# Kernel tuning notes

Measured on AMD Instinct MI355X. Metric: run time of the kernel, lower is better.

The kernel has to match this reference:

```python
import jax, jax.numpy as jnp
import numpy as np

SLOPE = 25.0  # snntorch surrogate.fast_sigmoid default slope
THR = 1.0
BETA = 0.5
NUM_HEADS = 8

@jax.custom_vjp
def spike(u):
    # forward: heaviside; backward: fast-sigmoid surrogate
    return (u > 0).astype(u.dtype)

def _spike_fwd(u):
    return (u > 0).astype(u.dtype), u

def _spike_bwd(u, g):
    return (g / (SLOPE * jnp.abs(u) + 1.0) ** 2,)

spike.defvjp(_spike_fwd, _spike_bwd)

def lif(inp, mem):
    # snntorch Leaky, reset_mechanism='subtract': reset from previous mem (detached)
    reset = jax.lax.stop_gradient((mem > THR).astype(mem.dtype))
    mem_new = BETA * mem + inp - reset * THR
    spk = spike(mem_new - THR)
    return spk, mem_new

def conv1x1(x, W):
    # nn.Conv2d(C,C,1,bias=False): pure channel matmul
    return jnp.einsum('bihw,oi->bohw', x, W)

def setup_inputs():
    key = jax.random.key(0)
    ks = jax.random.split(key, 5)
    B, C, H, W = 8, 256, 64, 64
    x = jax.random.normal(ks[0], (B, C, H, W), jnp.float32)
    z = jnp.zeros((B, C, H, W), jnp.float32)
    s = 1.0 / np.sqrt(C)
    Wq = jax.random.normal(ks[1], (C, C), jnp.float32) * s
    Wk = jax.random.normal(ks[2], (C, C), jnp.float32) * s
    Wv = jax.random.normal(ks[3], (C, C), jnp.float32) * s
    Wo = jax.random.normal(ks[4], (C, C), jnp.float32) * s
    gamma = jnp.ones((C,), jnp.float32)
    beta_bn = jnp.zeros((C,), jnp.float32)
    return {'x': x, 'q_mem': z, 'k_mem': z, 'v_mem': z,
            'Wq': Wq, 'Wk': Wk, 'Wv': Wv, 'Wo': Wo,
            'gamma': gamma, 'beta_bn': beta_bn}

def reference(x, q_mem, k_mem, v_mem, Wq, Wk, Wv, Wo, gamma, beta_bn):
    B, C, H, W = x.shape
    N = H * W
    hd = C // NUM_HEADS
    scale = hd ** -0.5

    q_spk, q_mem_n = lif(conv1x1(x, Wq), q_mem)
    k_spk, k_mem_n = lif(conv1x1(x, Wk), k_mem)
    v_spk, v_mem_n = lif(conv1x1(x, Wv), v_mem)

    # bipolar spikes in {-1,+1}, reshape to (B, h, N, d)
    def to_heads(s):
        t = (2.0 * s - 1.0).reshape(B, NUM_HEADS, hd, N)
        return jnp.transpose(t, (0, 1, 3, 2))

    q = jax.nn.elu(to_heads(q_spk)) + 1.0
    k = jax.nn.elu(to_heads(k_spk)) + 1.0
    v = to_heads(v_spk)

    kv = jnp.einsum('bhnd,bhne->bhde', k, v)            # (B,h,d,d)
    out = jnp.einsum('bhnd,bhde->bhne', q, kv) * scale  # (B,h,N,d)
    k_sum = jnp.sum(k, axis=2)                          # (B,h,d)
    denom = jnp.einsum('bhnd,bhd->bhn', q, k_sum) + 1e-6
    out = out / denom[..., None]

    out = jnp.transpose(out, (0, 1, 3, 2)).reshape(B, C, H, W)
    out = conv1x1(out, Wo)

    # BatchNorm2d, training mode (biased batch stats), eps=1e-5
    mean = jnp.mean(out, axis=(0, 2, 3), keepdims=True)
    var = jnp.var(out, axis=(0, 2, 3), keepdims=True)
    out = (out - mean) / jnp.sqrt(var + 1e-5)
    out = out * gamma[None, :, None, None] + beta_bn[None, :, None, None]

    return (out, q_mem_n, k_mem_n, v_mem_n)
```

## Files before the change

### kernel.cpp

```cpp
#include <hip/hip_runtime.h>

#define B_ 8
#define C_ 256
#define N_ 4096
#define HD_ 32

#define ALPHA_ 0.36787944117144233f
#define BETAS_ (2.0f - ALPHA_)
#define SCALE_ 0.17677669529663687f

typedef _Float16 f16;
typedef _Float16 f16x8 __attribute__((ext_vector_type(8)));
typedef float f32x4 __attribute__((ext_vector_type(4)));
typedef unsigned long long u64;
typedef __attribute__((address_space(3))) f16 lds_f16;

#define MFMA(a,b,c) __builtin_amdgcn_mfma_f32_16x16x32_f16((a),(b),(c),0,0,0)

#define GLDS(g, l) __builtin_amdgcn_global_load_lds( \
    (const __attribute__((address_space(1))) void*)(g), \
    (__attribute__((address_space(3))) void*)(l), 16, 0, 0)

#define DSR(dst, off) asm volatile("ds_read_b128 %0, %1" : "=v"(dst) : "v"(off))

template<int N> __device__ __forceinline__ void wait_vmcnt() {
    if constexpr (N == 0)       asm volatile("s_waitcnt vmcnt(0)" ::: "memory");
    else if constexpr (N == 2)  asm volatile("s_waitcnt vmcnt(2)" ::: "memory");
    else if constexpr (N == 4)  asm volatile("s_waitcnt vmcnt(4)" ::: "memory");
    else if constexpr (N == 8)  asm volatile("s_waitcnt vmcnt(8)" ::: "memory");
    else if constexpr (N == 16) asm volatile("s_waitcnt vmcnt(16)" ::: "memory");
}

__global__ __launch_bounds__(256) void transpose_split(
    const float* __restrict__ x, f16* __restrict__ XTh, f16* __restrict__ XTl)
{
    __shared__ float tile[32][257];
    int t = threadIdx.x;
    int b = blockIdx.z, i0 = blockIdx.y * 32, n0 = blockIdx.x * 256;
    const float* src = x + ((size_t)b * C_ + i0) * N_ + n0;
    int r = t >> 3, c0 = (t & 7) * 32;
    #pragma unroll
    for (int q = 0; q < 8; ++q) {
        float4 v = *reinterpret_cast<const float4*>(src + (size_t)r * N_ + c0 + q * 4);
        tile[r][c0 + q*4 + 0] = v.x; tile[r][c0 + q*4 + 1] = v.y;
        tile[r][c0 + q*4 + 2] = v.z; tile[r][c0 + q*4 + 3] = v.w;
    }
    __syncthreads();
    size_t ob = ((size_t)b * N_ + n0 + t) * C_ + i0;
    #pragma unroll
    for (int q = 0; q < 4; ++q) {
        f16x8 hv, lv;
        #pragma unroll
        for (int j = 0; j < 8; ++j) {
            float v = tile[q*8 + j][t];
            f16 h = (f16)v;
            hv[j] = h;
            lv[j] = (f16)(v - (float)h);
        }
        *reinterpret_cast<f16x8*>(XTh + ob + q*8) = hv;
        *reinterpret_cast<f16x8*>(XTl + ob + q*8) = lv;
    }
}

__global__ __launch_bounds__(256) void weight_split(
    const float* __restrict__ Wq, const float* __restrict__ Wk,
    const float* __restrict__ Wv, const float* __restrict__ Wo,
    f16* __restrict__ Wch, f16* __restrict__ Wcl)
{
    int idx4 = (blockIdx.x * 256 + threadIdx.x) * 4;
    int o = idx4 >> 8, i = idx4 & 255;
    const float* src = (o < 256) ? (Wq + (size_t)o * 256)
                     : (o < 512) ? (Wk + (size_t)(o - 256) * 256)
                     : (o < 768) ? (Wv + (size_t)(o - 512) * 256)
                                 : (Wo + (size_t)(o - 768) * 256);
    float4 v = *reinterpret_cast<const float4*>(src + i);
    f16 h0 = (f16)v.x, h1 = (f16)v.y, h2 = (f16)v.z, h3 = (f16)v.w;
    f16 hh[4] = { h0, h1, h2, h3 };
    f16 ll[4] = { (f16)(v.x - (float)h0), (f16)(v.y - (float)h1),
                  (f16)(v.z - (float)h2), (f16)(v.w - (float)h3) };
    *reinterpret_cast<uint2*>(Wch + idx4) = *reinterpret_cast<uint2*>(hh);
    *reinterpret_cast<uint2*>(Wcl + idx4) = *reinterpret_cast<uint2*>(ll);
}

template<bool LIF, bool FULLP>
__global__ __launch_bounds__(256, 3) void mfma_gemm(
    const f16* __restrict__ Wch, const f16* __restrict__ Wcl,
    const f16* __restrict__ Bh,  const f16* __restrict__ Bl,
    const float* __restrict__ mq, const float* __restrict__ mk2,
    const float* __restrict__ mv,
    float* __restrict__ o0, float* __restrict__ o1, float* __restrict__ o2,
    u64* __restrict__ rowAll)
{
    constexpr int SLOTS = FULLP ? 1024 : 512;
    constexpr int NGL   = FULLP ? 4 : 2;

    int gid = blockIdx.x;
    int b = gid & 7, slot = gid >> 3;
    int conv, oTi, nt;
    if (LIF) { conv = slot % 3; int rest = slot / 3; oTi = rest & 1; nt = rest >> 1; }
    else     { conv = 0;        oTi = slot & 1;      nt = slot >> 1; }
    int wRow0 = (LIF ? conv * 256 : 768) + oTi * 128;
    int chOut0 = oTi * 128;
    int nT = nt * 128;

    const float* memP = nullptr; float* outP; u64* rowP = nullptr;
    if (LIF) {
        memP = (conv == 0) ? mq : (conv == 1) ? mk2 : mv;
        outP = (conv == 0) ? o0 : (conv == 1) ? o1 : o2;
        rowP = rowAll + (size_t)conv * (8 * 256 * 64);
    } else outP = o0;

    __shared__ __align__(16) f16 smem[3][SLOTS * 8];

    int t = threadIdx.x;
    int wid = t >> 6, lane = t & 63;
    int wm = wid >> 1, wn = wid & 1;
    int lr = lane & 15, g = lane >> 4;

    const f16* gB[NGL];
    #pragma unroll
    for (int i = 0; i < NGL; ++i) {
        int s = i * 256 + t;
        int sp = s & 511;
        int r = sp >> 2, c = (sp & 3) ^ ((r >> 1) & 3);
        const f16* plane = (s < 512) ? Bh : Bl;
        gB[i] = plane + ((size_t)b * N_ + nT + r) * 256 + c * 8;
    }

    int aOff[4];
    #pragma unroll
    for (int m = 0; m < 4; ++m)
        aOff[m] = (wRow0 + wm * 64 + m * 16 + lr) * 256 + g * 8;

    unsigned lbase = (unsigned)(size_t)(lds_f16*)&smem[0][0];
    unsigned offB[4];
    #pragma unroll
    for (int n = 0; n < 4; ++n) {
        int r = wn * 64 + n * 16 + lr;
        offB[n] = (unsigned)((r * 4 + (g ^ ((r >> 1) & 3))) * 16);
    }

    f32x4 acc[4][4];
    #pragma unroll
    for (int m = 0; m < 4; ++m)
        #pragma unroll
        for (int n = 0; n < 4; ++n) acc[m][n] = (f32x4){0.f, 0.f, 0.f, 0.f};

    #pragma unroll
    for (int i = 0; i < NGL; ++i) GLDS(gB[i],      &smem[0][(i * 256 + t) * 8]);
    #pragma unroll
    for (int i = 0; i < NGL; ++i) GLDS(gB[i] + 32, &smem[1][(i * 256 + t) * 8]);
    wait_vmcnt<NGL>();
    __builtin_amdgcn_s_barrier();
    __builtin_amdgcn_sched_barrier(0);

#define GEMM_STEP(KS) do { \
    constexpr int ks = (KS); \
    f16x8 ah[4], al[4]; \
    _Pragma("unroll") \
    for (int m = 0; m < 4; ++m) { \
        ah[m] = *reinterpret_cast<const f16x8*>(Wch + aOff[m] + ks * 32); \
        if (FULLP) al[m] = *reinterpret_cast<const f16x8*>(Wcl + aOff[m] + ks * 32); \
    } \
    __builtin_amdgcn_sched_barrier(0); \
    if constexpr (ks < 6) { \
        _Pragma("unroll") \
        for (int i = 0; i < NGL; ++i) \
            GLDS(gB[i] + (ks + 2) * 32, &smem[(ks + 2) % 3][(i * 256 + t) * 8]); \
    } \
    __builtin_amdgcn_sched_barrier(0); \
    const unsigned base = lbase + (unsigned)((ks % 3) * (SLOTS * 16)); \
    f16x8 bhf[4], blf[4]; \
    _Pragma("unroll") \
    for (int n = 0; n < 4; ++n) { \
        DSR(bhf[n], base + offB[n]); \
        if (FULLP) DSR(blf[n], base + offB[n] + 8192); \
    } \
    asm volatile("s_waitcnt lgkmcnt(0)" ::: "memory"); \
    __builtin_amdgcn_sched_barrier(0); \
    wait_vmcnt<(ks < 6) ? (FULLP ? 4 : 2) : 0>();   \
    __builtin_amdgcn_sched_barrier(0); \
    _Pragma("unroll") \
    for (int n = 0; n < 4; ++n) \
        _Pragma("unroll") \
        for (int m = 0; m < 4; ++m) { \
            acc[m][n] = MFMA(ah[m], bhf[n], acc[m][n]); \
            if (FULLP) { \
                acc[m][n] = MFMA(ah[m], blf[n], acc[m][n]); \
                acc[m][n] = MFMA(al[m], bhf[n], acc[m][n]); \
            } \
        } \
    __builtin_amdgcn_sched_barrier(0); \
    __builtin_amdgcn_s_barrier(); \
    __builtin_amdgcn_sched_barrier(0); \
} while (0)

    GEMM_STEP(0); GEMM_STEP(1); GEMM_STEP(2); GEMM_STEP(3);
    GEMM_STEP(4); GEMM_STEP(5); GEMM_STEP(6); GEMM_STEP(7);
#undef GEMM_STEP

    if (LIF) {
        #pragma unroll
        for (int m = 0; m < 4; ++m) {
            int oLoc = chOut0 + wm * 64 + m * 16 + g * 4;
            u64 rw0 = 0, rw1 = 0, rw2 = 0, rw3 = 0;
            #pragma unroll
            for (int n = 0; n < 4; ++n) {
                int nn = nT + wn * 64 + n * 16 + lr;
                #pragma unroll
                for (int r = 0; r < 4; ++r) {
                    size_t idx = ((size_t)b * C_ + oLoc + r) * N_ + nn;
                    float mm = memP[idx];
                    float v = 0.5f * mm + acc[m][n][r] - (mm > 1.0f ? 1.0f : 0.0f);
                    outP[idx] = v;
                    u64 bl = __ballot(v > 1.0f);
                    u64 fld = ((bl >> (g * 16)) & 0xFFFFull) << (n * 16);
                    if (r == 0) rw0 |= fld; else if (r == 1) rw1 |= fld;
                    else if (r == 2) rw2 |= fld; else rw3 |= fld;
                }
            }
            if (lr == 0) {
                size_t rb = ((size_t)b * 256 + oLoc) * 64 + (nt * 2 + wn);
                rowP[rb]       = rw0;
                rowP[rb + 64]  = rw1;
                rowP[rb + 128] = rw2;
                rowP[rb + 192] = rw3;
            }
        }
    } else {
        #pragma unroll
        for (int m = 0; m < 4; ++m) {
            int oLoc = chOut0 + wm * 64 + m * 16 + g * 4;
            #pragma unroll
            for (int n = 0; n < 4; ++n) {
                int nn = nT + wn * 64 + n * 16 + lr;
                #pragma unroll
                for (int r = 0; r < 4; ++r) {
                    size_t idx = ((size_t)b * C_ + oLoc + r) * N_ + nn;
                    outP[idx] = acc[m][n][r];
                }
            }
        }
    }
}

__global__ __launch_bounds__(256) void kv_stage1(
    const u64* __restrict__ krow, const u64* __restrict__ vrow,
    int* __restrict__ pkv, int* __restrict__ pck, int* __restrict__ pcv)
{
    int bh = blockIdx.x, sl = blockIdx.y;
    int b = bh >> 3, h = bh & 7;
    __shared__ u64 kr[32][9], vr[32][9];
    int t = threadIdx.x;
    {
        int d = t >> 3, w = t & 7;
        size_t a = ((size_t)b * 256 + h * HD_ + d) * 64 + sl * 8 + w;
        kr[d][w] = krow[a];
        vr[d][w] = vrow[a];
    }
    __syncthreads();

    int base = bh * 8 + sl;
    if (t < 32) {
        int c = 0;
        #pragma unroll
        for (int w = 0; w < 8; ++w) c += __popcll(kr[t][w]);
        pck[base * 32 + t] = c;
    } else if (t < 64) {
        int dd = t - 32, c = 0;
        #pragma unroll
        for (int w = 0; w < 8; ++w) c += __popcll(vr[dd][w]);
        pcv[base * 32 + dd] = c;
    }
    int d = t >> 3, e0 = (t & 7) * 4;
    #pragma unroll
    for (int j = 0; j < 4; ++j) {
        int e = e0 + j, P = 0;
        #pragma unroll
        for (int w = 0; w < 8; ++w) P += __popcll(kr[d][w] & vr[e][w]);
        pkv[(size_t)base * 1024 + d * 32 + e] = P;
    }
}

__global__ __launch_bounds__(256) void kv_stage2(
    const int* __restrict__ pkv, const int* __restrict__ pck,
    const int* __restrict__ pcv, float* __restrict__ kvp, float* __restrict__ ksump)
{
    int bh = blockIdx.x, t = threadIdx.x;
    __shared__ float ck[32], cv[32];
    if (t < 32) {
        int s = 0;
        #pragma unroll
        for (int sl = 0; sl < 8; ++sl) s += pck[(bh * 8 + sl) * 32 + t];
        ck[t] = (float)s;
    } else if (t < 64) {
        int dd = t - 32, s = 0;
        #pragma unroll
        for (int sl = 0; sl < 8; ++sl) s += pcv[(bh * 8 + sl) * 32 + dd];
        cv[dd] = (float)s;
    }
    __syncthreads();
    int d = t >> 3, e0 = (t & 7) * 4;
    #pragma unroll
    for (int j = 0; j < 4; ++j) {
        int e = e0 + j, P = 0;
        #pragma unroll
        for (int sl = 0; sl < 8; ++sl) P += pkv[(size_t)(bh * 8 + sl) * 1024 + d * 32 + e];
        float skv = 2.0f * (float)P - ck[d];
        float sv  = 2.0f * cv[e] - 4096.0f;
        kvp[(size_t)bh * 1024 + d * 32 + e] = ALPHA_ * sv + BETAS_ * skv;
    }
    if ((t & 7) == 0)
        ksump[bh * 32 + d] = ALPHA_ * 4096.0f + BETAS_ * ck[d];
}

__global__ __launch_bounds__(256) void att_kernel(
    const u64* __restrict__ qrow, const float* __restrict__ kvp,
    const float* __restrict__ ksump, f16* __restrict__ ATh)
{
    int bh = blockIdx.y; int b = bh >> 3, h = bh & 7;
    int n0 = blockIdx.x * 256;

    __shared__ u64 qw[32][5];
    int t = threadIdx.x;
    if (t < 128) {
        int d2 = t >> 2, w4 = t & 3;
        qw[d2][w4] = qrow[((size_t)b * 256 + h * HD_ + d2) * 64 + (n0 >> 6) + w4];
    }
    __syncthreads();

    float q[32];
    #pragma unroll
    for (int d2 = 0; d2 < 32; ++d2)
        q[d2] = ((qw[d2][t >> 6] >> (t & 63)) & 1) ? 2.0f : ALPHA_;

    const float* ksb = ksump + bh * 32;
    float den = 1e-6f;
    #pragma unroll
    for (int d2 = 0; d2 < 32; ++d2) den += q[d2] * ksb[d2];
    float rden = SCALE_ / den;

    const float* kvb = kvp + (size_t)bh * 1024;
    size_t ob = ((size_t)b * N_ + n0 + t) * C_ + h * HD_;
    #pragma unroll
    for (int qq = 0; qq < 4; ++qq) {
        f16x8 hv;
        #pragma unroll
        for (int j = 0; j < 8; ++j) {
            int e = qq * 8 + j;
            float num = 0.0f;
            #pragma unroll
            for (int d2 = 0; d2 < 32; ++d2) num += q[d2] * kvb[d2 * 32 + e];
            hv[j] = (f16)(num * rden);
        }
        *reinterpret_cast<f16x8*>(ATh + ob + qq * 8) = hv;
    }
}

__global__ __launch_bounds__(1024) void bn_stats(
    const float* __restrict__ out2, float* __restrict__ stats)
{
    int o = blockIdx.x, t = threadIdx.x;
    double s = 0.0, ss = 0.0;
    for (int b = 0; b < B_; ++b) {
        const float* p = out2 + ((size_t)b * C_ + o) * N_;
        float4 v = *reinterpret_cast<const float4*>(&p[t * 4]);
        s  += (double)v.x + (double)v.y + (double)v.z + (double)v.w;
        ss += (double)v.x * v.x + (double)v.y * v.y + (double)v.z * v.z + (double)v.w * v.w;
    }
    __shared__ double rs[1024], rss[1024];
    rs[t] = s; rss[t] = ss;
    __syncthreads();
    for (int st = 512; st > 0; st >>= 1) {
        if (t < st) { rs[t] += rs[t + st]; rss[t] += rss[t + st]; }
        __syncthreads();
    }
    if (t == 0) {
        double mean = rs[0] / 32768.0;
        double var  = rss[0] / 32768.0 - mean * mean;
        stats[o * 2 + 0] = (float)mean;
        stats[o * 2 + 1] = (float)(1.0 / sqrt(var + 1e-5));
    }
}

__global__ __launch_bounds__(256) void bn_apply(
    float* __restrict__ out, const float* __restrict__ stats,
    const float* __restrict__ gamma, const float* __restrict__ beta)
{
    size_t i = ((size_t)blockIdx.x * 256 + threadIdx.x) * 4;
    int o = (int)((i >> 12) & 255);
    float m = stats[o * 2], r = stats[o * 2 + 1];
    float g = gamma[o] * r;
    float c = beta[o] - m * g;
    float4 v = *reinterpret_cast<float4*>(&out[i]);
    v.x = v.x * g + c; v.y = v.y * g + c;
    v.z = v.z * g + c; v.w = v.w * g + c;
    *reinterpret_cast<float4*>(&out[i]) = v;
}

extern "C" void kernel_launch(void* const* d_in, const int* in_sizes, int n_in,
                              void* d_out, int out_size, void* d_ws, size_t ws_size,
                              hipStream_t stream)
{
    (void)in_sizes; (void)n_in; (void)out_size; (void)ws_size;

    const float* x     = (const float*)d_in[0];
    const float* qmem  = (const float*)d_in[1];
    const float* kmem  = (const float*)d_in[2];
    const float* vmem  = (const float*)d_in[3];
    const float* Wq    = (const float*)d_in[4];
    const float* Wk    = (const float*)d_in[5];
    const float* Wv    = (const float*)d_in[6];
    const float* Wo    = (const float*)d_in[7];
    const float* gamma = (const float*)d_in[8];
    const float* beta  = (const float*)d_in[9];

    const size_t TSZ = (size_t)B_ * C_ * N_;
    float* out0 = (float*)d_out;
    float* outq = out0 + TSZ;
    float* outk = outq + TSZ;
    float* outv = outk + TSZ;

    const size_t RSZ = (size_t)8 * 256 * 64;
    char* w = (char*)d_ws;
    f16* XTh = (f16*)w;           w += TSZ * 2;
    f16* XTl = (f16*)w;           w += TSZ * 2;
    f16* ATh = (f16*)w;           w += TSZ * 2;
    f16* Wch = (f16*)w;           w += 1024 * 256 * 2;
    f16* Wcl = (f16*)w;           w += 1024 * 256 * 2;
    u64* rowm = (u64*)w;          w += 3 * RSZ * 8;
    int* pkv = (int*)w;           w += 64 * 8 * 1024 * 4;
    int* pck = (int*)w;           w += 64 * 8 * 32 * 4;
    int* pcv = (int*)w;           w += 64 * 8 * 32 * 4;
    float* kvp   = (float*)w;     w += 64 * 1024 * 4;
    float* ksump = (float*)w;     w += 64 * 32 * 4;
    float* stats = (float*)w;     w += 256 * 2 * 4;

    dim3 blk(256);

    transpose_split<<<dim3(16, 8, 8), blk, 0, stream>>>(x, XTh, XTl);
    weight_split<<<dim3(256), blk, 0, stream>>>(Wq, Wk, Wv, Wo, Wch, Wcl);

    mfma_gemm<true, true><<<dim3(1536), blk, 0, stream>>>(
        Wch, Wcl, XTh, XTl, qmem, kmem, vmem, outq, outk, outv, rowm);

    kv_stage1<<<dim3(64, 8), blk, 0, stream>>>(rowm + RSZ, rowm + 2 * RSZ, pkv, pck, pcv);
    kv_stage2<<<dim3(64), blk, 0, stream>>>(pkv, pck, pcv, kvp, ksump);

    att_kernel<<<dim3(16, 64), blk, 0, stream>>>(rowm, kvp, ksump, ATh);

    mfma_gemm<false, false><<<dim3(512), blk, 0, stream>>>(
        Wch, Wcl, ATh, ATh, nullptr, nullptr, nullptr, out0, nullptr, nullptr, nullptr);

    bn_stats<<<dim3(256), dim3(1024), 0, stream>>>(out0, stats);
    bn_apply<<<dim3(8192), blk, 0, stream>>>(out0, stats, gamma, beta);
}
```

Measured before the change: 184.8 us.

## Prefetch weight fragments one k-step ahead with double-buffered register loads

Weight (A) fragments were loaded synchronously from global memory at the start of each k-step. They are now loaded via inline-asm global_load_dwordx4 one step ahead into double-buffered registers, and the vmcnt waits are recounted so the A loads overlap with the LDS-staged B loads and the MFMAs. The extra register buffers raise pressure, so the occupancy hint drops from 3 to 2 blocks per SM, which risks less latency hiding from other waves. The final barrier is also dropped on the last step.

```diff
diff --git a/kernel.cpp b/kernel.cpp
--- a/kernel.cpp
+++ b/kernel.cpp
@@ -23,11 +23,17 @@
 
 #define DSR(dst, off) asm volatile("ds_read_b128 %0, %1" : "=v"(dst) : "v"(off))
 
+#define GLA(dst, ptr, ofs) asm volatile( \
+    "global_load_dwordx4 %0, %1, off offset:%c2" \
+    : "=v"(dst) : "v"(ptr), "i"(ofs))
+
 template<int N> __device__ __forceinline__ void wait_vmcnt() {
     if constexpr (N == 0)       asm volatile("s_waitcnt vmcnt(0)" ::: "memory");
     else if constexpr (N == 2)  asm volatile("s_waitcnt vmcnt(2)" ::: "memory");
     else if constexpr (N == 4)  asm volatile("s_waitcnt vmcnt(4)" ::: "memory");
+    else if constexpr (N == 6)  asm volatile("s_waitcnt vmcnt(6)" ::: "memory");
     else if constexpr (N == 8)  asm volatile("s_waitcnt vmcnt(8)" ::: "memory");
+    else if constexpr (N == 12) asm volatile("s_waitcnt vmcnt(12)" ::: "memory");
     else if constexpr (N == 16) asm volatile("s_waitcnt vmcnt(16)" ::: "memory");
 }
 
@@ -83,7 +89,7 @@
 }
 
 template<bool LIF, bool FULLP>
-__global__ __launch_bounds__(256, 3) void mfma_gemm(
+__global__ __launch_bounds__(256, 2) void mfma_gemm(
     const f16* __restrict__ Wch, const f16* __restrict__ Wcl,
     const f16* __restrict__ Bh,  const f16* __restrict__ Bl,
     const float* __restrict__ mq, const float* __restrict__ mk2,
@@ -93,6 +99,7 @@
 {
     constexpr int SLOTS = FULLP ? 1024 : 512;
     constexpr int NGL   = FULLP ? 4 : 2;
+    constexpr int NA    = FULLP ? 8 : 4;
 
     int gid = blockIdx.x;
     int b = gid & 7, slot = gid >> 3;
@@ -127,10 +134,13 @@
         gB[i] = plane + ((size_t)b * N_ + nT + r) * 256 + c * 8;
     }
 
-    int aOff[4];
-    #pragma unroll
-    for (int m = 0; m < 4; ++m)
-        aOff[m] = (wRow0 + wm * 64 + m * 16 + lr) * 256 + g * 8;
+    const f16* aPh[4]; const f16* aPl[4];
+    #pragma unroll
+    for (int m = 0; m < 4; ++m) {
+        int off = (wRow0 + wm * 64 + m * 16 + lr) * 256 + g * 8;
+        aPh[m] = Wch + off;
+        aPl[m] = Wcl + off;
+    }
 
     unsigned lbase = (unsigned)(size_t)(lds_f16*)&smem[0][0];
     unsigned offB[4];
@@ -146,8 +156,15 @@
         #pragma unroll
         for (int n = 0; n < 4; ++n) acc[m][n] = (f32x4){0.f, 0.f, 0.f, 0.f};
 
-    #pragma unroll
-    for (int i = 0; i < NGL; ++i) GLDS(gB[i],      &smem[0][(i * 256 + t) * 8]);
+    f16x8 aH[2][4], aL[2][4];
+
+    #pragma unroll
+    for (int i = 0; i < NGL; ++i) GLDS(gB[i], &smem[0][(i * 256 + t) * 8]);
+    #pragma unroll
+    for (int m = 0; m < 4; ++m) {
+        GLA(aH[0][m], aPh[m], 0);
+        if (FULLP) GLA(aL[0][m], aPl[m], 0);
+    }
     #pragma unroll
     for (int i = 0; i < NGL; ++i) GLDS(gB[i] + 32, &smem[1][(i * 256 + t) * 8]);
     wait_vmcnt<NGL>();
@@ -156,19 +173,8 @@
 
 #define GEMM_STEP(KS) do { \
     constexpr int ks = (KS); \
-    f16x8 ah[4], al[4]; \
-    _Pragma("unroll") \
-    for (int m = 0; m < 4; ++m) { \
-        ah[m] = *reinterpret_cast<const f16x8*>(Wch + aOff[m] + ks * 32); \
-        if (FULLP) al[m] = *reinterpret_cast<const f16x8*>(Wcl + aOff[m] + ks * 32); \
-    } \
-    __builtin_amdgcn_sched_barrier(0); \
-    if constexpr (ks < 6) { \
-        _Pragma("unroll") \
-        for (int i = 0; i < NGL; ++i) \
-            GLDS(gB[i] + (ks + 2) * 32, &smem[(ks + 2) % 3][(i * 256 + t) * 8]); \
-    } \
-    __builtin_amdgcn_sched_barrier(0); \
+    constexpr int cur = ks & 1, nxt = (ks + 1) & 1; \
+     \
     const unsigned base = lbase + (unsigned)((ks % 3) * (SLOTS * 16)); \
     f16x8 bhf[4], blf[4]; \
     _Pragma("unroll") \
@@ -176,23 +182,45 @@
         DSR(bhf[n], base + offB[n]); \
         if (FULLP) DSR(blf[n], base + offB[n] + 8192); \
     } \
+    __builtin_amdgcn_sched_barrier(0); \
+     \
+    if constexpr (ks < 7) { \
+        _Pragma("unroll") \
+        for (int m = 0; m < 4; ++m) { \
+            GLA(aH[nxt][m], aPh[m], (ks + 1) * 64); \
+            if (FULLP) GLA(aL[nxt][m], aPl[m], (ks + 1) * 64); \
+        } \
+    } \
+    __builtin_amdgcn_sched_barrier(0); \
+     \
+    if constexpr (ks < 6) { \
+        _Pragma("unroll") \
+        for (int i = 0; i < NGL; ++i) \
+            GLDS(gB[i] + (ks + 2) * 32, &smem[(ks + 2) % 3][(i * 256 + t) * 8]); \
+    } \
+    __builtin_amdgcn_sched_barrier(0); \
     asm volatile("s_waitcnt lgkmcnt(0)" ::: "memory"); \
     __builtin_amdgcn_sched_barrier(0); \
-    wait_vmcnt<(ks < 6) ? (FULLP ? 4 : 2) : 0>();   \
+     \
+    wait_vmcnt<(ks <= 5) ? (2 * NGL + NA) : (ks == 6 ? (NGL + NA) : 0)>(); \
     __builtin_amdgcn_sched_barrier(0); \
     _Pragma("unroll") \
     for (int n = 0; n < 4; ++n) \
         _Pragma("unroll") \
         for (int m = 0; m < 4; ++m) { \
-            acc[m][n] = MFMA(ah[m], bhf[n], acc[m][n]); \
+            acc[m][n] = MFMA(aH[cur][m], bhf[n], acc[m][n]); \
             if (FULLP) { \
-                acc[m][n] = MFMA(ah[m], blf[n], acc[m][n]); \
-                acc[m][n] = MFMA(al[m], bhf[n], acc[m][n]); \
+                acc[m][n] = MFMA(aH[cur][m], blf[n], acc[m][n]); \
+                acc[m][n] = MFMA(aL[cur][m], bhf[n], acc[m][n]); \
             } \
         } \
     __builtin_amdgcn_sched_barrier(0); \
-    __builtin_amdgcn_s_barrier(); \
-    __builtin_amdgcn_sched_barrier(0); \
+    if constexpr (ks < 7) { \
+         \
+        wait_vmcnt<(ks <= 5) ? (NA + NGL) : NA>(); \
+        __builtin_amdgcn_s_barrier(); \
+        __builtin_amdgcn_sched_barrier(0); \
+    } \
 } while (0)
 
     GEMM_STEP(0); GEMM_STEP(1); GEMM_STEP(2); GEMM_STEP(3);
```

Measured after the change: 174.6 us. 5.5% less time.
